# Optimization experiments

Hardware: AMD Instinct MI355X
Metric: run time of the kernel (lower is better)

## Reference

```python
import jax, jax.numpy as jnp
import numpy as np

N, IN_C, OUT_C = 8192, 256, 256


def setup_inputs() -> dict:
    key = jax.random.key(0)
    k1, k2, k3 = jax.random.split(key, 3)
    x = jax.random.normal(k1, (N, IN_C), dtype=jnp.float32)
    adj = jax.random.uniform(k2, (N, N), dtype=jnp.float32)
    # learned parameter: torch.rand(in_channels, out_channels)
    w = jax.random.uniform(k3, (IN_C, OUT_C), dtype=jnp.float32)
    return {"x": x, "adj": adj, "w": w}


def reference(x, adj, w):
    # A = adj + I
    A = adj + jnp.eye(adj.shape[0], dtype=adj.dtype)
    # D_hat = sqrt(inv(diag(rowsum(A)))) == diag(deg^{-1/2}) since D is diagonal
    deg = jnp.sum(A, axis=1)                      # [N]
    d_isqrt = jax.lax.rsqrt(deg)                  # [N]
    # A_hat = D_hat @ A @ D_hat  ==  row/col scaling by d^{-1/2}
    A_hat = A * d_isqrt[:, None] * d_isqrt[None, :]
    # ELU((A_hat @ x) @ w)
    h = jnp.matmul(A_hat, x)                      # [N, in_c]
    return jax.nn.elu(jnp.matmul(h, w))           # [N, out_c]
```

## Files before the change

### kernel.cpp

```cpp
#include <hip/hip_runtime.h>
#include <stdint.h>

#define N_NODES 8192
#define CH 256
#define MT 32
#define BK 64
#define KB_COUNT (N_NODES / BK)

typedef __bf16 bf16x8 __attribute__((ext_vector_type(8)));
typedef float f32x4 __attribute__((ext_vector_type(4)));
typedef unsigned int u32x4 __attribute__((ext_vector_type(4)));

__device__ __forceinline__ void async_copy16(const void* g, void* l) {
  __builtin_amdgcn_global_load_lds(
      (const __attribute__((address_space(1))) void*)(uintptr_t)g,
      (__attribute__((address_space(3))) void*)(uint32_t)(uintptr_t)l,
      16, 0, 0);
}

__device__ __forceinline__ unsigned short f32_to_bf16_rne(float f) {
  unsigned u = __float_as_uint(f);
  u += 0x7FFFu + ((u >> 16) & 1u);
  return (unsigned short)(u >> 16);
}

__global__ void __launch_bounds__(256) k_deg(const float* __restrict__ adj,
                                             float* __restrict__ dsq) {
  __shared__ float red[256];
  const int row = blockIdx.x;
  const f32x4* ar = (const f32x4*)(adj + (size_t)row * N_NODES);
  float s = 0.f;
#pragma unroll
  for (int i = 0; i < 8; ++i) {
    f32x4 v = ar[threadIdx.x + 256 * i];
    s += (v.x + v.y) + (v.z + v.w);
  }
  red[threadIdx.x] = s;
  __syncthreads();
  for (int st = 128; st > 0; st >>= 1) {
    if (threadIdx.x < (unsigned)st) red[threadIdx.x] += red[threadIdx.x + st];
    __syncthreads();
  }
  if (threadIdx.x == 0) dsq[row] = rsqrtf(red[0] + 1.0f);
}

__global__ void __launch_bounds__(256) k_ytrans(const float* __restrict__ x,
                                                const float* __restrict__ dsq,
                                                unsigned short* __restrict__ yt) {
  __shared__ float tile[64][65];
  __shared__ float ds_s[64];
  const int j0 = blockIdx.x * 64, c0 = blockIdx.y * 64;
  const int t = threadIdx.x;
  const int lc = t & 63, lr4 = t >> 6;
  if (t < 64) ds_s[t] = dsq[j0 + t];
  __syncthreads();
#pragma unroll
  for (int rr = 0; rr < 16; ++rr) {
    int jr = rr * 4 + lr4;
    tile[jr][lc] = x[(size_t)(j0 + jr) * CH + c0 + lc] * ds_s[jr];
  }
  __syncthreads();
#pragma unroll
  for (int rr = 0; rr < 16; ++rr) {
    int cr = rr * 4 + lr4;
    yt[(size_t)(c0 + cr) * N_NODES + j0 + lc] = f32_to_bf16_rne(tile[lc][cr]);
  }
}

__global__ void __launch_bounds__(256, 1) k_gemm1(const float* __restrict__ adj,
                                                  const unsigned short* __restrict__ yt,
                                                  const float* __restrict__ x,
                                                  const float* __restrict__ dsq,
                                                  float* __restrict__ hout) {
  __shared__ __align__(16) float As[2][MT * BK];
  __shared__ __align__(16) unsigned short Bs[2][CH * BK];

  const int tid = threadIdx.x;
  const int wave = tid >> 6;
  const int lane = tid & 63;
  const int m0 = blockIdx.x * MT;
  const int lr = lane & 15;
  const int lq = lane >> 4;

  const float* ag[2];
  int aoffu[2];
#pragma unroll
  for (int q = 0; q < 2; ++q) {
    int i = wave * 2 + q;
    int s = 64 * i + lane;
    int row = s >> 4;
    int c16 = (lane & 15) ^ (row & 15);
    ag[q] = adj + (size_t)(m0 + row) * N_NODES + c16 * 4;
    aoffu[q] = 64 * i * 16;
  }
  const unsigned short* bg[8];
  int boffu[8];
#pragma unroll
  for (int q = 0; q < 8; ++q) {
    int i = wave * 8 + q;
    int s = 64 * i + lane;
    int n = s >> 3;
    int c8 = (lane & 7) ^ (n & 7);
    bg[q] = yt + (size_t)n * N_NODES + c8 * 8;
    boffu[q] = 64 * i * 16;
  }

  f32x4 acc[2][4];
#pragma unroll
  for (int i = 0; i < 2; ++i)
#pragma unroll
    for (int j = 0; j < 4; ++j) acc[i][j] = (f32x4){0.f, 0.f, 0.f, 0.f};

  auto issue = [&](int b, int k0) {
    char* aL = (char*)&As[b][0];
    char* bL = (char*)&Bs[b][0];
#pragma unroll
    for (int q = 0; q < 2; ++q) async_copy16(ag[q] + k0, aL + aoffu[q]);
#pragma unroll
    for (int q = 0; q < 8; ++q) async_copy16(bg[q] + k0, bL + boffu[q]);
  };

  issue(0, 0);

  for (int kb = 0; kb < KB_COUNT; ++kb) {
    const int b = kb & 1;
    if (kb + 1 < KB_COUNT) {
      issue(b ^ 1, (kb + 1) * BK);
      asm volatile("s_waitcnt vmcnt(10)\n\ts_barrier" ::: "memory");
    } else {
      asm volatile("s_waitcnt vmcnt(0)\n\ts_barrier" ::: "memory");
    }

    const char* aB = (const char*)&As[b][0];
    const char* bB = (const char*)&Bs[b][0];

#pragma unroll
    for (int k32 = 0; k32 < 2; ++k32) {
      bf16x8 afr[2];
#pragma unroll
      for (int mt = 0; mt < 2; ++mt) {
        int row = mt * 16 + lr;
        int c16 = k32 * 8 + lq * 2;
        int s0 = row * 16 + ((c16) ^ (row & 15));
        int s1 = row * 16 + ((c16 + 1) ^ (row & 15));
        f32x4 r0 = *(const f32x4*)(aB + s0 * 16);
        f32x4 r1 = *(const f32x4*)(aB + s1 * 16);
        u32x4 pk;
        pk.x = __builtin_amdgcn_perm(__float_as_uint(r0.y), __float_as_uint(r0.x), 0x07060302u);
        pk.y = __builtin_amdgcn_perm(__float_as_uint(r0.w), __float_as_uint(r0.z), 0x07060302u);
        pk.z = __builtin_amdgcn_perm(__float_as_uint(r1.y), __float_as_uint(r1.x), 0x07060302u);
        pk.w = __builtin_amdgcn_perm(__float_as_uint(r1.w), __float_as_uint(r1.z), 0x07060302u);
        afr[mt] = __builtin_bit_cast(bf16x8, pk);
      }
#pragma unroll
      for (int nt = 0; nt < 4; ++nt) {
        int n = wave * 64 + nt * 16 + lr;
        int c8 = k32 * 4 + lq;
        int s = n * 8 + (c8 ^ (n & 7));
        bf16x8 bfr = *(const bf16x8*)(bB + s * 16);
        acc[0][nt] = __builtin_amdgcn_mfma_f32_16x16x32_bf16(afr[0], bfr, acc[0][nt], 0, 0, 0);
        acc[1][nt] = __builtin_amdgcn_mfma_f32_16x16x32_bf16(afr[1], bfr, acc[1][nt], 0, 0, 0);
      }
    }
    asm volatile("s_waitcnt lgkmcnt(0)\n\ts_barrier" ::: "memory");
  }

#pragma unroll
  for (int mt = 0; mt < 2; ++mt) {
#pragma unroll
    for (int r = 0; r < 4; ++r) {
      int row = m0 + mt * 16 + lq * 4 + r;
      float di = dsq[row];
#pragma unroll
      for (int nt = 0; nt < 4; ++nt) {
        int col = wave * 64 + nt * 16 + lr;
        float v = acc[mt][nt][r];
        v = di * (v + di * x[(size_t)row * CH + col]);
        hout[(size_t)row * CH + col] = v;
      }
    }
  }
}

__global__ void __launch_bounds__(256) k_gemm2(float* __restrict__ h,
                                               const float* __restrict__ w) {
  __shared__ __align__(16) float hs[16][CH];
  const int r0 = blockIdx.x * 16;
  const int t = threadIdx.x;
#pragma unroll
  for (int i = 0; i < 16; ++i) hs[i][t] = h[(size_t)(r0 + i) * CH + t];
  __syncthreads();
  float acc[16];
#pragma unroll
  for (int r = 0; r < 16; ++r) acc[r] = 0.f;
  for (int k = 0; k < CH; k += 4) {
    float w0 = w[(k + 0) * CH + t];
    float w1 = w[(k + 1) * CH + t];
    float w2 = w[(k + 2) * CH + t];
    float w3 = w[(k + 3) * CH + t];
#pragma unroll
    for (int r = 0; r < 16; ++r) {
      f32x4 hv = *(const f32x4*)&hs[r][k];
      acc[r] += hv.x * w0 + hv.y * w1 + hv.z * w2 + hv.w * w3;
    }
  }
#pragma unroll
  for (int r = 0; r < 16; ++r) {
    float v = acc[r];
    v = v > 0.f ? v : expm1f(v);
    h[(size_t)(r0 + r) * CH + t] = v;
  }
}

extern "C" void kernel_launch(void* const* d_in, const int* in_sizes, int n_in,
                              void* d_out, int out_size, void* d_ws, size_t ws_size,
                              hipStream_t stream) {
  const float* x = (const float*)d_in[0];
  const float* adj = (const float*)d_in[1];
  const float* w = (const float*)d_in[2];
  float* out = (float*)d_out;

  float* dsq = (float*)d_ws;
  unsigned short* yt = (unsigned short*)((char*)d_ws + 32768);

  k_deg<<<N_NODES, 256, 0, stream>>>(adj, dsq);
  k_ytrans<<<dim3(N_NODES / 64, CH / 64), 256, 0, stream>>>(x, dsq, yt);
  k_gemm1<<<N_NODES / MT, 256, 0, stream>>>(adj, yt, x, dsq, out);
  k_gemm2<<<N_NODES / 16, 256, 0, stream>>>(out, w);
}
```

Baseline: 507.8 us.

## Reassociate to multiply x by W first and fuse ELU into adjacency GEMM

Computes Z = X·W before the big adjacency GEMM, so the second small GEMM kernel disappears and ELU is applied in the GEMM1 epilogue. The new kernel also writes the degree-scaled, transposed bf16 copy of Z used as the B operand, replacing the separate transpose kernel. The degree kernel now reduces one row per wave with shuffles instead of a shared-memory tree. The GEMM main loop swaps the hand-tuned vmcnt/barrier asm for a plain __syncthreads before issuing the next prefetch, which may weaken overlap of loads with compute. Z is rounded to bf16, which changes rounding behaviour.

```diff
diff --git a/kernel.cpp b/kernel.cpp
--- a/kernel.cpp
+++ b/kernel.cpp
@@ -6,6 +6,7 @@
 #define MT 32
 #define BK 64
 #define KB_COUNT (N_NODES / BK)
+#define ZROWS 16
 
 typedef __bf16 bf16x8 __attribute__((ext_vector_type(8)));
 typedef float f32x4 __attribute__((ext_vector_type(4)));
@@ -26,52 +27,63 @@
 
 __global__ void __launch_bounds__(256) k_deg(const float* __restrict__ adj,
                                              float* __restrict__ dsq) {
-  __shared__ float red[256];
-  const int row = blockIdx.x;
+  const int wave = threadIdx.x >> 6, lane = threadIdx.x & 63;
+  const int row = blockIdx.x * 4 + wave;
   const f32x4* ar = (const f32x4*)(adj + (size_t)row * N_NODES);
-  float s = 0.f;
+  float s0 = 0.f, s1 = 0.f, s2 = 0.f, s3 = 0.f;
 #pragma unroll
   for (int i = 0; i < 8; ++i) {
-    f32x4 v = ar[threadIdx.x + 256 * i];
-    s += (v.x + v.y) + (v.z + v.w);
-  }
-  red[threadIdx.x] = s;
+    f32x4 a = ar[lane + 64 * (4 * i + 0)];
+    f32x4 b = ar[lane + 64 * (4 * i + 1)];
+    f32x4 c = ar[lane + 64 * (4 * i + 2)];
+    f32x4 d = ar[lane + 64 * (4 * i + 3)];
+    s0 += (a.x + a.y) + (a.z + a.w);
+    s1 += (b.x + b.y) + (b.z + b.w);
+    s2 += (c.x + c.y) + (c.z + c.w);
+    s3 += (d.x + d.y) + (d.z + d.w);
+  }
+  float s = (s0 + s1) + (s2 + s3);
+#pragma unroll
+  for (int off = 32; off > 0; off >>= 1) s += __shfl_down(s, off, 64);
+  if (lane == 0) dsq[row] = rsqrtf(s + 1.0f);
+}
+
+__global__ void __launch_bounds__(256) k_zy(const float* __restrict__ x,
+                                            const float* __restrict__ w,
+                                            const float* __restrict__ dsq,
+                                            float* __restrict__ z,
+                                            unsigned short* __restrict__ yt) {
+  __shared__ float xs[ZROWS][CH];
+  const int r0 = blockIdx.x * ZROWS;
+  const int t = threadIdx.x;
+#pragma unroll
+  for (int r = 0; r < ZROWS; ++r) xs[r][t] = x[(size_t)(r0 + r) * CH + t];
   __syncthreads();
-  for (int st = 128; st > 0; st >>= 1) {
-    if (threadIdx.x < (unsigned)st) red[threadIdx.x] += red[threadIdx.x + st];
-    __syncthreads();
-  }
-  if (threadIdx.x == 0) dsq[row] = rsqrtf(red[0] + 1.0f);
-}
-
-__global__ void __launch_bounds__(256) k_ytrans(const float* __restrict__ x,
-                                                const float* __restrict__ dsq,
-                                                unsigned short* __restrict__ yt) {
-  __shared__ float tile[64][65];
-  __shared__ float ds_s[64];
-  const int j0 = blockIdx.x * 64, c0 = blockIdx.y * 64;
-  const int t = threadIdx.x;
-  const int lc = t & 63, lr4 = t >> 6;
-  if (t < 64) ds_s[t] = dsq[j0 + t];
-  __syncthreads();
-#pragma unroll
-  for (int rr = 0; rr < 16; ++rr) {
-    int jr = rr * 4 + lr4;
-    tile[jr][lc] = x[(size_t)(j0 + jr) * CH + c0 + lc] * ds_s[jr];
-  }
-  __syncthreads();
-#pragma unroll
-  for (int rr = 0; rr < 16; ++rr) {
-    int cr = rr * 4 + lr4;
-    yt[(size_t)(c0 + cr) * N_NODES + j0 + lc] = f32_to_bf16_rne(tile[lc][cr]);
-  }
+  float acc[ZROWS];
+#pragma unroll
+  for (int r = 0; r < ZROWS; ++r) acc[r] = 0.f;
+  for (int k = 0; k < CH; k += 8) {
+    float wv[8];
+#pragma unroll
+    for (int u = 0; u < 8; ++u) wv[u] = w[(size_t)(k + u) * CH + t];
+#pragma unroll
+    for (int r = 0; r < ZROWS; ++r) {
+#pragma unroll
+      for (int u = 0; u < 8; ++u) acc[r] += xs[r][k + u] * wv[u];
+    }
+  }
+#pragma unroll
+  for (int r = 0; r < ZROWS; ++r) z[(size_t)(r0 + r) * CH + t] = acc[r];
+#pragma unroll
+  for (int r = 0; r < ZROWS; ++r)
+    yt[(size_t)t * N_NODES + r0 + r] = f32_to_bf16_rne(dsq[r0 + r] * acc[r]);
 }
 
 __global__ void __launch_bounds__(256, 1) k_gemm1(const float* __restrict__ adj,
                                                   const unsigned short* __restrict__ yt,
-                                                  const float* __restrict__ x,
+                                                  const float* __restrict__ z,
                                                   const float* __restrict__ dsq,
-                                                  float* __restrict__ hout) {
+                                                  float* __restrict__ out) {
   __shared__ __align__(16) float As[2][MT * BK];
   __shared__ __align__(16) unsigned short Bs[2][CH * BK];
 
@@ -124,12 +136,8 @@
 
   for (int kb = 0; kb < KB_COUNT; ++kb) {
     const int b = kb & 1;
-    if (kb + 1 < KB_COUNT) {
-      issue(b ^ 1, (kb + 1) * BK);
-      asm volatile("s_waitcnt vmcnt(10)\n\ts_barrier" ::: "memory");
-    } else {
-      asm volatile("s_waitcnt vmcnt(0)\n\ts_barrier" ::: "memory");
-    }
+    __syncthreads();
+    if (kb + 1 < KB_COUNT) issue(b ^ 1, (kb + 1) * BK);
 
     const char* aB = (const char*)&As[b][0];
     const char* bB = (const char*)&Bs[b][0];
@@ -162,7 +170,6 @@
         acc[1][nt] = __builtin_amdgcn_mfma_f32_16x16x32_bf16(afr[1], bfr, acc[1][nt], 0, 0, 0);
       }
     }
-    asm volatile("s_waitcnt lgkmcnt(0)\n\ts_barrier" ::: "memory");
   }
 
 #pragma unroll
@@ -175,40 +182,11 @@
       for (int nt = 0; nt < 4; ++nt) {
         int col = wave * 64 + nt * 16 + lr;
         float v = acc[mt][nt][r];
-        v = di * (v + di * x[(size_t)row * CH + col]);
-        hout[(size_t)row * CH + col] = v;
+        v = di * (v + di * z[(size_t)row * CH + col]);
+        v = v > 0.f ? v : expm1f(v);
+        out[(size_t)row * CH + col] = v;
       }
     }
-  }
-}
-
-__global__ void __launch_bounds__(256) k_gemm2(float* __restrict__ h,
-                                               const float* __restrict__ w) {
-  __shared__ __align__(16) float hs[16][CH];
-  const int r0 = blockIdx.x * 16;
-  const int t = threadIdx.x;
-#pragma unroll
-  for (int i = 0; i < 16; ++i) hs[i][t] = h[(size_t)(r0 + i) * CH + t];
-  __syncthreads();
-  float acc[16];
-#pragma unroll
-  for (int r = 0; r < 16; ++r) acc[r] = 0.f;
-  for (int k = 0; k < CH; k += 4) {
-    float w0 = w[(k + 0) * CH + t];
-    float w1 = w[(k + 1) * CH + t];
-    float w2 = w[(k + 2) * CH + t];
-    float w3 = w[(k + 3) * CH + t];
-#pragma unroll
-    for (int r = 0; r < 16; ++r) {
-      f32x4 hv = *(const f32x4*)&hs[r][k];
-      acc[r] += hv.x * w0 + hv.y * w1 + hv.z * w2 + hv.w * w3;
-    }
-  }
-#pragma unroll
-  for (int r = 0; r < 16; ++r) {
-    float v = acc[r];
-    v = v > 0.f ? v : expm1f(v);
-    h[(size_t)(r0 + r) * CH + t] = v;
   }
 }
 
@@ -222,9 +200,9 @@
 
   float* dsq = (float*)d_ws;
   unsigned short* yt = (unsigned short*)((char*)d_ws + 32768);
-
-  k_deg<<<N_NODES, 256, 0, stream>>>(adj, dsq);
-  k_ytrans<<<dim3(N_NODES / 64, CH / 64), 256, 0, stream>>>(x, dsq, yt);
-  k_gemm1<<<N_NODES / MT, 256, 0, stream>>>(adj, yt, x, dsq, out);
-  k_gemm2<<<N_NODES / 16, 256, 0, stream>>>(out, w);
-}
+  float* z = (float*)((char*)d_ws + 32768 + (size_t)CH * N_NODES * 2);
+
+  k_deg<<<N_NODES / 4, 256, 0, stream>>>(adj, dsq);
+  k_zy<<<N_NODES / ZROWS, 256, 0, stream>>>(x, w, dsq, z, yt);
+  k_gemm1<<<N_NODES / MT, 256, 0, stream>>>(adj, yt, z, dsq, out);
+}
```

Result: slower. 524.5 us (+3.3%).
